# Performance work log

Measured on AMD Instinct MI355X. Metric: run time of the kernel, lower is better.

## Reference

```python
import jax, jax.numpy as jnp
import numpy as np

BN, SN = 16, 64
C, T, FY, FX = 480, 8, 28, 28
OS = 8            # roialign output_size
NDF = 256
K = 64            # n_clusters
ALPHA = 1.0
IMG_W, IMG_H = 1920.0, 1080.0
SPATIAL_SCALE = 1.0


def _roi_align(feat, boxes):
    """torchvision RoIAlign with sampling_ratio=1, aligned=True.
    feat: [bn, C, H, W]; boxes: [bn, sn, 4] (x1,y1,x2,y2) in feature coords.
    Returns [bn, sn, C, OS, OS]."""
    bn, c, H, W = feat.shape
    xy1 = boxes[..., 0:2] * SPATIAL_SCALE - 0.5   # aligned=True offset
    xy2 = boxes[..., 2:4] * SPATIAL_SCALE - 0.5
    bin_wh = (xy2 - xy1) / OS                     # [bn,sn,2]
    ctr = jnp.arange(OS, dtype=feat.dtype) + 0.5  # one sample per bin (ratio=1)
    xs = xy1[..., 0:1] + ctr * bin_wh[..., 0:1]   # [bn,sn,OS]
    ys = xy1[..., 1:2] + ctr * bin_wh[..., 1:2]
    X = xs[:, :, None, :]                         # [bn,sn,1,OS]
    Y = ys[:, :, :, None]                         # [bn,sn,OS,1]
    valid = (Y > -1.0) & (Y < H) & (X > -1.0) & (X < W)
    x = jnp.clip(X, 0.0, W - 1.0)
    y = jnp.clip(Y, 0.0, H - 1.0)
    x0 = jnp.floor(x).astype(jnp.int32)
    y0 = jnp.floor(y).astype(jnp.int32)
    x1 = jnp.minimum(x0 + 1, W - 1)
    y1 = jnp.minimum(y0 + 1, H - 1)
    lx = x - x0
    ly = y - y0
    fhw = jnp.transpose(feat, (0, 2, 3, 1))       # [bn,H,W,C]
    g = jax.vmap(lambda f, yy, xx: f[yy, xx])     # broadcasting gather -> [bn,sn,OS,OS,C]
    v00 = g(fhw, y0, x0); v01 = g(fhw, y0, x1)
    v10 = g(fhw, y1, x0); v11 = g(fhw, y1, x1)
    wy0, wy1 = (1.0 - ly)[..., None], ly[..., None]
    wx0, wx1 = (1.0 - lx)[..., None], lx[..., None]
    out = v00 * wy0 * wx0 + v01 * wy0 * wx1 + v10 * wy1 * wx0 + v11 * wy1 * wx1
    out = jnp.where(valid[..., None], out, 0.0)
    return jnp.transpose(out, (0, 1, 4, 2, 3))    # [bn,sn,C,OS,OS] (torch layout)


def setup_inputs() -> dict:
    key = jax.random.key(0)
    ks = jax.random.split(key, 6)
    z_vis = jax.random.normal(ks[0], (BN, C, T, FY, FX), jnp.float32)
    # valid boxes (x1<x2, y1<y2), fully inside the image -> no NaN padding rows
    tl = jax.random.uniform(ks[1], (BN, SN, 2)) * jnp.array([IMG_W * 0.5, IMG_H * 0.5])
    wh = jax.random.uniform(ks[2], (BN, SN, 2)) * jnp.array([IMG_W * 0.4, IMG_H * 0.4]) + 16.0
    bboxs = jnp.concatenate([tl, tl + wh], axis=-1).astype(jnp.float32)
    W_vis = jax.random.normal(ks[3], (C * OS * OS, NDF), jnp.float32) / np.sqrt(C * OS * OS)
    b_vis = jnp.zeros((NDF,), jnp.float32)
    W_spc = jax.random.normal(ks[4], (1, NDF), jnp.float32)
    b_spc = jnp.zeros((NDF,), jnp.float32)
    centroids = jax.random.normal(ks[5], (K, NDF), jnp.float32) * 0.1
    return {"z_vis": z_vis, "bboxs": bboxs, "W_vis": W_vis, "b_vis": b_vis,
            "W_spc": W_spc, "b_spc": b_spc, "centroids": centroids}


def reference(z_vis, bboxs, W_vis, b_vis, W_spc, b_spc, centroids):
    bn, sn = bboxs.shape[:2]
    # scale image-coord boxes to feature-map coords
    scale = jnp.array([FX / IMG_W, FY / IMG_H], dtype=z_vis.dtype)
    boxes_f = (bboxs.reshape(bn, sn, 2, 2) * scale).reshape(bn, sn, 4)
    feat = z_vis[:, :, -1]                                   # last temporal frame [bn,C,fy,fx]
    roi = _roi_align(feat, boxes_f).reshape(bn, sn, -1)      # [bn,sn,C*OS*OS]
    z_v = roi @ W_vis + b_vis                                # visual embedding [bn,sn,NDF]
    # spatial embedding: normalized distance of bbox center to image center (detached)
    b2 = bboxs.reshape(bn, sn, 2, 2)
    ctr = b2[:, :, 0] + (b2[:, :, 1] - b2[:, :, 0]) * 0.5    # [bn,sn,2]
    img_c = jnp.array([IMG_W / 2.0, IMG_H / 2.0], dtype=z_vis.dtype)
    norms = jnp.linalg.norm(ctr - img_c, axis=-1, keepdims=True) / jnp.linalg.norm(img_c)
    norms = jax.lax.stop_gradient(norms)                     # .detach() in original
    z_s = norms @ W_spc + b_spc                              # [bn,sn,NDF]
    z = z_v + z_s
    # Student-t soft assignment on L2 distance (NOT squared, as in the source)
    d = jnp.linalg.norm(z[:, :, None, :] - centroids, axis=-1)   # [bn,sn,K]
    s_un = (1.0 + d / ALPHA) ** (-(ALPHA + 1.0) / 2.0)
    s = s_un / jnp.sum(s_un, axis=-1, keepdims=True)
    c = jnp.argmax(s, axis=-1)
    return z, s, c
```

## Files before the change

### kernel.cpp

```cpp
#include <hip/hip_runtime.h>
#include <cstdint>
#include <cstddef>

#define BN_   16
#define C_    480
#define T_    8
#define FY_   28
#define FX_   28
#define NDF_  256
#define KC_   64
#define M_    1024
#define KD_   30720
#define PLANE_ 784
#define CHSTRIDE_ (T_*PLANE_)
#define CT_   (C_*CHSTRIDE_)
#define KS_   32
#define KCH_  960
#define NCH_  15
#define MT_   32
#define APAD_ 72

typedef __attribute__((ext_vector_type(8))) short bf16x8;
typedef __attribute__((ext_vector_type(4))) float f32x4;

__device__ __forceinline__ unsigned rne_bf16(float f) {
    union { float f; unsigned u; } v; v.f = f;
    return v.u + 0x7FFFu + ((v.u >> 16) & 1u);
}
__device__ __forceinline__ float bfbits_to_f(unsigned r) {
    union { unsigned u; float f; } v; v.u = r & 0xFFFF0000u;
    return v.f;
}

__global__ __launch_bounds__(256)
void convert_w(const float* __restrict__ W, unsigned short* __restrict__ Wt_hi,
               unsigned short* __restrict__ Wt_lo) {
    __shared__ unsigned short th[64][68];
    __shared__ unsigned short tl[64][68];
    const int k0 = blockIdx.x * 64, n0 = blockIdx.y * 64;
    const int t = threadIdx.x;
    const int sub = t >> 4, off4 = (t & 15) * 4;
    #pragma unroll
    for (int p = 0; p < 4; ++p) {
        const int kr = p * 16 + sub;
        const float4 v = *(const float4*)&W[(size_t)(k0 + kr) * NDF_ + n0 + off4];
        const float vv[4] = { v.x, v.y, v.z, v.w };
        #pragma unroll
        for (int e = 0; e < 4; ++e) {
            const unsigned rh = rne_bf16(vv[e]);
            const unsigned rl = rne_bf16(vv[e] - bfbits_to_f(rh));
            th[kr][off4 + e] = (unsigned short)(rh >> 16);
            tl[kr][off4 + e] = (unsigned short)(rl >> 16);
        }
    }
    __syncthreads();
    #pragma unroll
    for (int p = 0; p < 4; ++p) {
        const int nr = p * 16 + sub;
        ushort4 oh, ol;
        oh.x = th[off4 + 0][nr]; oh.y = th[off4 + 1][nr];
        oh.z = th[off4 + 2][nr]; oh.w = th[off4 + 3][nr];
        ol.x = tl[off4 + 0][nr]; ol.y = tl[off4 + 1][nr];
        ol.z = tl[off4 + 2][nr]; ol.w = tl[off4 + 3][nr];
        *(ushort4*)&Wt_hi[(size_t)(n0 + nr) * KD_ + k0 + off4] = oh;
        *(ushort4*)&Wt_lo[(size_t)(n0 + nr) * KD_ + k0 + off4] = ol;
    }
}

__global__ void convert_cent(const float* __restrict__ cent, float* __restrict__ centT) {
    const int k = blockIdx.x;
    const int j = threadIdx.x;
    centT[(size_t)j * KC_ + k] = cent[(size_t)k * NDF_ + j];
}

__global__ __launch_bounds__(256, 3)
void gemm_fused(const float* __restrict__ z_vis, const unsigned short* __restrict__ Wt_hi,
                const unsigned short* __restrict__ Wt_lo, const float* __restrict__ bboxs,
                float* __restrict__ part) {
    __shared__ short Ah[MT_ * APAD_];
    __shared__ short Al[MT_ * APAD_];
    __shared__ unsigned short Bh[256 * 32];
    __shared__ unsigned short Bl[256 * 32];
    __shared__ float Pl[PLANE_];

    const int t = threadIdx.x;
    const int ks = blockIdx.x, mi = blockIdx.y;
    const int lane = t & 63, wid = t >> 6;
    const int kbase = ks * KCH_;

    const int m = t >> 3, by = t & 7;
    const int roi = mi * MT_ + m;
    const int bn = mi >> 1;

    int xi0[8], xi1[8];
    float xw0[8], xw1[8];
    int yr0, yr1;
    float wy0v, wy1v;
    {
        const float bx1 = bboxs[roi * 4 + 0], by1 = bboxs[roi * 4 + 1];
        const float bx2 = bboxs[roi * 4 + 2], by2 = bboxs[roi * 4 + 3];
        const float sx = 28.0f / 1920.0f, sy = 28.0f / 1080.0f;
        const float lo_x = bx1 * sx - 0.5f;
        const float binw_x = (bx2 * sx - 0.5f - lo_x) * 0.125f;
        const float lo_y = by1 * sy - 0.5f;
        const float binw_y = (by2 * sy - 0.5f - lo_y) * 0.125f;
        #pragma unroll
        for (int b = 0; b < 8; ++b) {
            const float pos = lo_x + ((float)b + 0.5f) * binw_x;
            const float vx = (pos > -1.0f && pos < 28.0f) ? 1.0f : 0.0f;
            const float pc = fminf(fmaxf(pos, 0.0f), 27.0f);
            const float p0 = floorf(pc);
            const float lx = pc - p0;
            xi0[b] = (int)p0;
            xi1[b] = min(xi0[b] + 1, 27);
            xw0[b] = vx * (1.0f - lx);
            xw1[b] = vx * lx;
        }
        const float pos = lo_y + ((float)by + 0.5f) * binw_y;
        const float vy = (pos > -1.0f && pos < 28.0f) ? 1.0f : 0.0f;
        const float pc = fminf(fmaxf(pos, 0.0f), 27.0f);
        const float p0 = floorf(pc);
        const float ly = pc - p0;
        const int y0 = (int)p0, y1 = min(y0 + 1, 27);
        yr0 = y0 * FX_; yr1 = y1 * FX_;
        wy0v = vy * (1.0f - ly); wy1v = vy * ly;
    }
    const float* plane = z_vis + (size_t)bn * CT_ + (size_t)(T_ - 1) * PLANE_;

    const int brow_l = lane >> 2;
    const int bkoff = (lane & 3) * 8;

    auto plane_load = [&](int cc) {
        if (wid != 0) return;
        const char* gb = (const char*)(plane + (size_t)(ks * NCH_ + cc) * CHSTRIDE_);
        #pragma unroll
        for (int i = 0; i < 3; ++i)
            __builtin_amdgcn_global_load_lds(
                (const __attribute__((address_space(1))) void*)(gb + (i * 64 + lane) * 16),
                (__attribute__((address_space(3))) void*)((char*)Pl + i * 1024), 16, 0, 0);
        if (lane < 4)
            __builtin_amdgcn_global_load_lds(
                (const __attribute__((address_space(1))) void*)(gb + (192 + lane) * 16),
                (__attribute__((address_space(3))) void*)((char*)Pl + 3072), 16, 0, 0);
    };

    auto stage_B = [&](int s) {
        #pragma unroll
        for (int qq = 0; qq < 4; ++qq) {
            const int rbase = qq * 64 + wid * 16;
            const size_t goff = (size_t)(rbase + brow_l) * KD_ + kbase + s * 32 + bkoff;
            __builtin_amdgcn_global_load_lds(
                (const __attribute__((address_space(1))) void*)(Wt_hi + goff),
                (__attribute__((address_space(3))) void*)&Bh[rbase * 32], 16, 0, 0);
            __builtin_amdgcn_global_load_lds(
                (const __attribute__((address_space(1))) void*)(Wt_lo + goff),
                (__attribute__((address_space(3))) void*)&Bl[rbase * 32], 16, 0, 0);
        }
    };

    auto stage_A = [&]() {
        unsigned rh[8], rl[8];
        #pragma unroll
        for (int b = 0; b < 8; ++b) {
            const float v00 = Pl[yr0 + xi0[b]], v01 = Pl[yr0 + xi1[b]];
            const float v10 = Pl[yr1 + xi0[b]], v11 = Pl[yr1 + xi1[b]];
            const float val = wy0v * (xw0[b] * v00 + xw1[b] * v01)
                            + wy1v * (xw0[b] * v10 + xw1[b] * v11);
            rh[b] = rne_bf16(val);
            rl[b] = rne_bf16(val - bfbits_to_f(rh[b]));
        }
        const uint4 hh = make_uint4(__builtin_amdgcn_perm(rh[1], rh[0], 0x07060302u),
                                    __builtin_amdgcn_perm(rh[3], rh[2], 0x07060302u),
                                    __builtin_amdgcn_perm(rh[5], rh[4], 0x07060302u),
                                    __builtin_amdgcn_perm(rh[7], rh[6], 0x07060302u));
        const uint4 ll = make_uint4(__builtin_amdgcn_perm(rl[1], rl[0], 0x07060302u),
                                    __builtin_amdgcn_perm(rl[3], rl[2], 0x07060302u),
                                    __builtin_amdgcn_perm(rl[5], rl[4], 0x07060302u),
                                    __builtin_amdgcn_perm(rl[7], rl[6], 0x07060302u));
        *(uint4*)&Ah[m * APAD_ + by * 8] = hh;
        *(uint4*)&Al[m * APAD_ + by * 8] = ll;
    };

    const int fr = lane & 15, fq = lane >> 4;
    f32x4 acc[2][4] = {};

    plane_load(0);
    stage_B(0);
    __syncthreads();
    stage_A();

    for (int cc = 0; cc < NCH_; ++cc) {
        #pragma unroll
        for (int half = 0; half < 2; ++half) {
            const int s = 2 * cc + half;
            __syncthreads();

            bf16x8 afh[2], afl[2], bh[4], bl[4];
            #pragma unroll
            for (int i = 0; i < 2; ++i) {
                afh[i] = *(const bf16x8*)&Ah[(i * 16 + fr) * APAD_ + half * 32 + fq * 8];
                afl[i] = *(const bf16x8*)&Al[(i * 16 + fr) * APAD_ + half * 32 + fq * 8];
            }
            #pragma unroll
            for (int j = 0; j < 4; ++j) {
                bh[j] = *(const bf16x8*)&Bh[(wid * 64 + j * 16 + fr) * 32 + fq * 8];
                bl[j] = *(const bf16x8*)&Bl[(wid * 64 + j * 16 + fr) * 32 + fq * 8];
            }
            __syncthreads();

            if (half == 0) {
                stage_B(s + 1);
                if (cc + 1 < NCH_) plane_load(cc + 1);
            } else if (cc + 1 < NCH_) {
                stage_B(s + 1);
                stage_A();
            }

            #pragma unroll
            for (int j = 0; j < 4; ++j)
                #pragma unroll
                for (int i = 0; i < 2; ++i) {
                    acc[i][j] = __builtin_amdgcn_mfma_f32_16x16x32_bf16(afh[i], bh[j], acc[i][j], 0, 0, 0);
                    acc[i][j] = __builtin_amdgcn_mfma_f32_16x16x32_bf16(afl[i], bh[j], acc[i][j], 0, 0, 0);
                    acc[i][j] = __builtin_amdgcn_mfma_f32_16x16x32_bf16(afh[i], bl[j], acc[i][j], 0, 0, 0);
                }
        }
    }

    float* pb = part + (size_t)ks * M_ * NDF_;
    #pragma unroll
    for (int i = 0; i < 2; ++i) {
        const int row = mi * MT_ + i * 16 + fq * 4;
        #pragma unroll
        for (int j = 0; j < 4; ++j) {
            const int col = wid * 64 + j * 16 + fr;
            #pragma unroll
            for (int r = 0; r < 4; ++r)
                pb[(size_t)(row + r) * NDF_ + col] = acc[i][j][r];
        }
    }
}

__global__ __launch_bounds__(256)
void cluster_kernel(const float* __restrict__ part, const float* __restrict__ bboxs,
                    const float* __restrict__ b_vis, const float* __restrict__ W_spc,
                    const float* __restrict__ b_spc, const float* __restrict__ centT,
                    float* __restrict__ out) {
    const int row = blockIdx.x, t = threadIdx.x;
    __shared__ float zs[NDF_];
    __shared__ float dp[4][KC_];

    float a = 0.0f;
    #pragma unroll
    for (int kp = 0; kp < KS_; ++kp)
        a += part[(size_t)kp * M_ * NDF_ + (size_t)row * NDF_ + t];

    const float x1 = bboxs[row * 4 + 0], y1 = bboxs[row * 4 + 1];
    const float x2 = bboxs[row * 4 + 2], y2 = bboxs[row * 4 + 3];
    const float cx = x1 + (x2 - x1) * 0.5f - 960.0f;
    const float cy = y1 + (y2 - y1) * 0.5f - 540.0f;
    const float nrm = sqrtf(cx * cx + cy * cy) / sqrtf(960.0f * 960.0f + 540.0f * 540.0f);

    const float zj = a + b_vis[t] + nrm * W_spc[t] + b_spc[t];
    zs[t] = zj;
    out[(size_t)row * NDF_ + t] = zj;
    __syncthreads();

    const int k = t & 63, qq = t >> 6;
    {
        float d2 = 0.0f;
        const float* ct = centT + (size_t)qq * 64 * KC_;
        #pragma unroll 8
        for (int j = 0; j < 64; ++j) {
            const float df = zs[qq * 64 + j] - ct[(size_t)j * KC_ + k];
            d2 += df * df;
        }
        dp[qq][k] = d2;
    }
    __syncthreads();

    if (t < 64) {
        const float d = sqrtf(dp[0][t] + dp[1][t] + dp[2][t] + dp[3][t]);
        const float su = 1.0f / (1.0f + d);
        float sum = su;
        #pragma unroll
        for (int mk = 1; mk < 64; mk <<= 1) sum += __shfl_xor(sum, mk, 64);
        out[(size_t)M_ * NDF_ + (size_t)row * KC_ + t] = su / sum;
        float v = d; int idx = t;
        #pragma unroll
        for (int mk = 1; mk < 64; mk <<= 1) {
            const float ov = __shfl_xor(v, mk, 64);
            const int oi = __shfl_xor(idx, mk, 64);
            if (ov < v || (ov == v && oi < idx)) { v = ov; idx = oi; }
        }
        if (t == 0)
            out[(size_t)M_ * NDF_ + (size_t)M_ * KC_ + row] = (float)idx;
    }
}

extern "C" void kernel_launch(void* const* d_in, const int* in_sizes, int n_in,
                              void* d_out, int out_size, void* d_ws, size_t ws_size,
                              hipStream_t stream) {
    const float* z_vis = (const float*)d_in[0];
    const float* bboxs = (const float*)d_in[1];
    const float* W_vis = (const float*)d_in[2];
    const float* b_vis = (const float*)d_in[3];
    const float* W_spc = (const float*)d_in[4];
    const float* b_spc = (const float*)d_in[5];
    const float* cent  = (const float*)d_in[6];
    float* out = (float*)d_out;

    char* ws = (char*)d_ws;
    unsigned short* Wt_hi = (unsigned short*)ws;
    unsigned short* Wt_lo = (unsigned short*)(ws + 15728640);
    float*          centT = (float*)(ws + 2 * 15728640);
    float*          part  = (float*)(ws + 2 * 15728640 + 65536);

    convert_w<<<dim3(KD_ / 64, NDF_ / 64), 256, 0, stream>>>(W_vis, Wt_hi, Wt_lo);
    convert_cent<<<KC_, 256, 0, stream>>>(cent, centT);
    gemm_fused<<<dim3(KS_, M_ / MT_), 256, 0, stream>>>(z_vis, Wt_hi, Wt_lo, bboxs, part);
    cluster_kernel<<<M_, 256, 0, stream>>>(part, bboxs, b_vis, W_spc, b_spc, centT, out);
}
```

Before: 408.3 us.

## Pack weights into per-step contiguous tiles and reduce split-K via atomics

```diff
diff --git a/kernel.cpp b/kernel.cpp
--- a/kernel.cpp
+++ b/kernel.cpp
@@ -17,8 +17,10 @@
 #define KS_   32
 #define KCH_  960
 #define NCH_  15
+#define NSTEP_ 30
 #define MT_   32
 #define APAD_ 72
+#define BTILE_ 16384
 
 typedef __attribute__((ext_vector_type(8))) short bf16x8;
 typedef __attribute__((ext_vector_type(4))) float f32x4;
@@ -33,37 +35,29 @@
 }
 
 __global__ __launch_bounds__(256)
-void convert_w(const float* __restrict__ W, unsigned short* __restrict__ Wt_hi,
-               unsigned short* __restrict__ Wt_lo) {
-    __shared__ unsigned short th[64][68];
-    __shared__ unsigned short tl[64][68];
-    const int k0 = blockIdx.x * 64, n0 = blockIdx.y * 64;
-    const int t = threadIdx.x;
-    const int sub = t >> 4, off4 = (t & 15) * 4;
+void convert_pack(const float* __restrict__ W, unsigned short* __restrict__ Bpack) {
+    const int blk = blockIdx.x;
+    const int kb = blk * 32;
+    const int n = threadIdx.x;
+    unsigned hw[16], lw[16];
     #pragma unroll
-    for (int p = 0; p < 4; ++p) {
-        const int kr = p * 16 + sub;
-        const float4 v = *(const float4*)&W[(size_t)(k0 + kr) * NDF_ + n0 + off4];
-        const float vv[4] = { v.x, v.y, v.z, v.w };
-        #pragma unroll
-        for (int e = 0; e < 4; ++e) {
-            const unsigned rh = rne_bf16(vv[e]);
-            const unsigned rl = rne_bf16(vv[e] - bfbits_to_f(rh));
-            th[kr][off4 + e] = (unsigned short)(rh >> 16);
-            tl[kr][off4 + e] = (unsigned short)(rl >> 16);
-        }
-    }
-    __syncthreads();
+    for (int p = 0; p < 16; ++p) {
+        const float v0 = W[(size_t)(kb + 2 * p) * NDF_ + n];
+        const float v1 = W[(size_t)(kb + 2 * p + 1) * NDF_ + n];
+        const unsigned h0 = rne_bf16(v0), h1 = rne_bf16(v1);
+        const unsigned l0 = rne_bf16(v0 - bfbits_to_f(h0));
+        const unsigned l1 = rne_bf16(v1 - bfbits_to_f(h1));
+        hw[p] = __builtin_amdgcn_perm(h1, h0, 0x07060302u);
+        lw[p] = __builtin_amdgcn_perm(l1, l0, 0x07060302u);
+    }
+    unsigned short* hb = Bpack + (size_t)blk * BTILE_;
+    unsigned short* lb = hb + 8192;
+    uint4* ho = (uint4*)hb + n * 4;
+    uint4* lo = (uint4*)lb + n * 4;
     #pragma unroll
-    for (int p = 0; p < 4; ++p) {
-        const int nr = p * 16 + sub;
-        ushort4 oh, ol;
-        oh.x = th[off4 + 0][nr]; oh.y = th[off4 + 1][nr];
-        oh.z = th[off4 + 2][nr]; oh.w = th[off4 + 3][nr];
-        ol.x = tl[off4 + 0][nr]; ol.y = tl[off4 + 1][nr];
-        ol.z = tl[off4 + 2][nr]; ol.w = tl[off4 + 3][nr];
-        *(ushort4*)&Wt_hi[(size_t)(n0 + nr) * KD_ + k0 + off4] = oh;
-        *(ushort4*)&Wt_lo[(size_t)(n0 + nr) * KD_ + k0 + off4] = ol;
+    for (int q = 0; q < 4; ++q) {
+        ho[q] = make_uint4(hw[q * 4 + 0], hw[q * 4 + 1], hw[q * 4 + 2], hw[q * 4 + 3]);
+        lo[q] = make_uint4(lw[q * 4 + 0], lw[q * 4 + 1], lw[q * 4 + 2], lw[q * 4 + 3]);
     }
 }
 
@@ -74,9 +68,8 @@
 }
 
 __global__ __launch_bounds__(256, 3)
-void gemm_fused(const float* __restrict__ z_vis, const unsigned short* __restrict__ Wt_hi,
-                const unsigned short* __restrict__ Wt_lo, const float* __restrict__ bboxs,
-                float* __restrict__ part) {
+void gemm_fused(const float* __restrict__ z_vis, const unsigned short* __restrict__ Bpack,
+                const float* __restrict__ bboxs, float* __restrict__ z_acc) {
     __shared__ short Ah[MT_ * APAD_];
     __shared__ short Al[MT_ * APAD_];
     __shared__ unsigned short Bh[256 * 32];
@@ -86,7 +79,6 @@
     const int t = threadIdx.x;
     const int ks = blockIdx.x, mi = blockIdx.y;
     const int lane = t & 63, wid = t >> 6;
-    const int kbase = ks * KCH_;
 
     const int m = t >> 3, by = t & 7;
     const int roi = mi * MT_ + m;
@@ -127,9 +119,6 @@
     }
     const float* plane = z_vis + (size_t)bn * CT_ + (size_t)(T_ - 1) * PLANE_;
 
-    const int brow_l = lane >> 2;
-    const int bkoff = (lane & 3) * 8;
-
     auto plane_load = [&](int cc) {
         if (wid != 0) return;
         const char* gb = (const char*)(plane + (size_t)(ks * NCH_ + cc) * CHSTRIDE_);
@@ -145,16 +134,16 @@
     };
 
     auto stage_B = [&](int s) {
+        const unsigned short* hb = Bpack + (size_t)(ks * NSTEP_ + s) * BTILE_;
         #pragma unroll
         for (int qq = 0; qq < 4; ++qq) {
-            const int rbase = qq * 64 + wid * 16;
-            const size_t goff = (size_t)(rbase + brow_l) * KD_ + kbase + s * 32 + bkoff;
+            const int off = (qq * 64 + wid * 16) * 32;
             __builtin_amdgcn_global_load_lds(
-                (const __attribute__((address_space(1))) void*)(Wt_hi + goff),
-                (__attribute__((address_space(3))) void*)&Bh[rbase * 32], 16, 0, 0);
+                (const __attribute__((address_space(1))) void*)(hb + off + lane * 8),
+                (__attribute__((address_space(3))) void*)&Bh[off], 16, 0, 0);
             __builtin_amdgcn_global_load_lds(
-                (const __attribute__((address_space(1))) void*)(Wt_lo + goff),
-                (__attribute__((address_space(3))) void*)&Bl[rbase * 32], 16, 0, 0);
+                (const __attribute__((address_space(1))) void*)(hb + 8192 + off + lane * 8),
+                (__attribute__((address_space(3))) void*)&Bl[off], 16, 0, 0);
         }
     };
 
@@ -227,7 +216,6 @@
         }
     }
 
-    float* pb = part + (size_t)ks * M_ * NDF_;
     #pragma unroll
     for (int i = 0; i < 2; ++i) {
         const int row = mi * MT_ + i * 16 + fq * 4;
@@ -236,13 +224,13 @@
             const int col = wid * 64 + j * 16 + fr;
             #pragma unroll
             for (int r = 0; r < 4; ++r)
-                pb[(size_t)(row + r) * NDF_ + col] = acc[i][j][r];
+                atomicAdd(&z_acc[(size_t)(row + r) * NDF_ + col], acc[i][j][r]);
         }
     }
 }
 
 __global__ __launch_bounds__(256)
-void cluster_kernel(const float* __restrict__ part, const float* __restrict__ bboxs,
+void cluster_kernel(const float* __restrict__ z_acc, const float* __restrict__ bboxs,
                     const float* __restrict__ b_vis, const float* __restrict__ W_spc,
                     const float* __restrict__ b_spc, const float* __restrict__ centT,
                     float* __restrict__ out) {
@@ -250,10 +238,7 @@
     __shared__ float zs[NDF_];
     __shared__ float dp[4][KC_];
 
-    float a = 0.0f;
-    #pragma unroll
-    for (int kp = 0; kp < KS_; ++kp)
-        a += part[(size_t)kp * M_ * NDF_ + (size_t)row * NDF_ + t];
+    const float a = z_acc[(size_t)row * NDF_ + t];
 
     const float x1 = bboxs[row * 4 + 0], y1 = bboxs[row * 4 + 1];
     const float x2 = bboxs[row * 4 + 2], y2 = bboxs[row * 4 + 3];
@@ -311,13 +296,13 @@
     float* out = (float*)d_out;
 
     char* ws = (char*)d_ws;
-    unsigned short* Wt_hi = (unsigned short*)ws;
-    unsigned short* Wt_lo = (unsigned short*)(ws + 15728640);
-    float*          centT = (float*)(ws + 2 * 15728640);
-    float*          part  = (float*)(ws + 2 * 15728640 + 65536);
-
-    convert_w<<<dim3(KD_ / 64, NDF_ / 64), 256, 0, stream>>>(W_vis, Wt_hi, Wt_lo);
+    unsigned short* Bpack = (unsigned short*)ws;
+    float*          centT = (float*)(ws + 31457280);
+    float*          z_acc = (float*)(ws + 31457280 + 65536);
+
+    convert_pack<<<KS_ * NSTEP_, 256, 0, stream>>>(W_vis, Bpack);
     convert_cent<<<KC_, 256, 0, stream>>>(cent, centT);
-    gemm_fused<<<dim3(KS_, M_ / MT_), 256, 0, stream>>>(z_vis, Wt_hi, Wt_lo, bboxs, part);
-    cluster_kernel<<<M_, 256, 0, stream>>>(part, bboxs, b_vis, W_spc, b_spc, centT, out);
-}
+    hipMemsetAsync(z_acc, 0, (size_t)M_ * NDF_ * sizeof(float), stream);
+    gemm_fused<<<dim3(KS_, M_ / MT_), 256, 0, stream>>>(z_vis, Bpack, bboxs, z_acc);
+    cluster_kernel<<<M_, 256, 0, stream>>>(z_acc, bboxs, b_vis, W_spc, b_spc, centT, out);
+}
```

Result: faster. 370.4 us (-9.3%).
